# Kernel optimization log

Hardware: AMD Instinct MI355X
Metric: run time of the kernel (lower is better)

The kernel has to match this reference:

```python
import jax, jax.numpy as jnp
import numpy as np


def setup_inputs() -> dict:
    B, C, D = 8192, 2048, 1024
    key = jax.random.key(0)
    kx, kc = jax.random.split(key)
    x = jax.random.normal(kx, (B, D), dtype=jnp.float32)
    # kaiming_normal_ init for centers: std = sqrt(2 / fan_in) with fan_in = feat_dim
    centers = jax.random.normal(kc, (C, D), dtype=jnp.float32) * jnp.sqrt(2.0 / D)
    sigma = jnp.ones((C, D), dtype=jnp.float32)  # nn.init.ones_
    return {"x": x, "centers": centers, "sigma": sigma}


def reference(x, centers, sigma):
    # Original loop computes, per class i:
    #   dist[:, i] = diag(m @ diag(sigma[i]) @ m.T)  with m = x - centers[i]
    # which equals sum_d sigma[i,d] * (x[b,d] - centers[i,d])^2.
    # Expand the square to avoid the O(B*C*D) broadcast intermediate:
    #   dist[b,i] = (x^2) @ sigma[i] - 2 * x @ (sigma[i]*centers[i]) + sum_d sigma[i,d]*centers[i,d]^2
    xsq_term = jnp.einsum('bd,id->bi', x * x, sigma)            # [B, C]
    cross = jnp.einsum('bd,id->bi', x, sigma * centers)          # [B, C]
    const = jnp.sum(sigma * centers * centers, axis=-1)          # [C]
    dist = xsq_term - 2.0 * cross + const[None, :]
    return (centers, sigma, -dist)
```

## Files before the change

### kernel.cpp

```cpp
#include <hip/hip_runtime.h>
#include <hip/hip_bf16.h>


#define B_SZ 8192
#define C_SZ 2048
#define D_SZ 1024
#define K2   2048
#define NT   32

typedef __attribute__((ext_vector_type(4))) float f32x4;
typedef __attribute__((ext_vector_type(8))) short bf16x8;

static __device__ __forceinline__ unsigned short f2bf(float f) {
  union { float f; unsigned int u; } v; v.f = f;
  unsigned int r = v.u + 0x7fffu + ((v.u >> 16) & 1u);
  return (unsigned short)(r >> 16);
}

__global__ __launch_bounds__(256) void build_a(const float* __restrict__ x,
                                               unsigned short* __restrict__ Aop) {
  const long t = (long)blockIdx.x * 256 + threadIdx.x;
  const long e = t * 8;
  const long b = e >> 10;
  const int  d = (int)(e & 1023);
  const float4* xv = (const float4*)x;
  float4 v0 = xv[2 * t], v1 = xv[2 * t + 1];
  float vs[8] = {v0.x, v0.y, v0.z, v0.w, v1.x, v1.y, v1.z, v1.w};
  unsigned short sq[8] __attribute__((aligned(16)));
  unsigned short rw[8] __attribute__((aligned(16)));
#pragma unroll
  for (int j = 0; j < 8; ++j) {
    rw[j] = f2bf(vs[j]);
    sq[j] = f2bf(vs[j] * vs[j]);
  }
  *(uint4*)(Aop + b * K2 + d)        = *(uint4*)sq;
  *(uint4*)(Aop + b * K2 + D_SZ + d) = *(uint4*)rw;
}

__global__ __launch_bounds__(128) void prep_w(const float* __restrict__ centers,
                                              const float* __restrict__ sigma,
                                              float* __restrict__ out_centers,
                                              float* __restrict__ out_sigma,
                                              unsigned short* __restrict__ Wop,
                                              float* __restrict__ cn) {
  const int i = blockIdx.x;
  const int t = threadIdx.x;
  const long base = (long)i * D_SZ;
  const float4* cv = (const float4*)(centers + base);
  const float4* sv = (const float4*)(sigma + base);
  float4 c0 = cv[2 * t], c1 = cv[2 * t + 1];
  float4 s0 = sv[2 * t], s1 = sv[2 * t + 1];
  ((float4*)(out_centers + base))[2 * t]     = c0;
  ((float4*)(out_centers + base))[2 * t + 1] = c1;
  ((float4*)(out_sigma + base))[2 * t]       = s0;
  ((float4*)(out_sigma + base))[2 * t + 1]   = s1;
  float cs[8] = {c0.x, c0.y, c0.z, c0.w, c1.x, c1.y, c1.z, c1.w};
  float ss[8] = {s0.x, s0.y, s0.z, s0.w, s1.x, s1.y, s1.z, s1.w};
  unsigned short w1[8] __attribute__((aligned(16)));
  unsigned short w2[8] __attribute__((aligned(16)));
  float p = 0.0f;
#pragma unroll
  for (int j = 0; j < 8; ++j) {
    w1[j] = f2bf(-ss[j]);
    w2[j] = f2bf(2.0f * ss[j] * cs[j]);
    p += ss[j] * cs[j] * cs[j];
  }
  *(uint4*)(Wop + (long)i * K2 + t * 8)        = *(uint4*)w1;
  *(uint4*)(Wop + (long)i * K2 + D_SZ + t * 8) = *(uint4*)w2;
#pragma unroll
  for (int off = 32; off > 0; off >>= 1) p += __shfl_down(p, off, 64);
  __shared__ float red[2];
  if ((t & 63) == 0) red[t >> 6] = p;
  __syncthreads();
  if (t == 0) cn[i] = -(red[0] + red[1]);
}

#define LGKM0() asm volatile("s_waitcnt lgkmcnt(0)" ::: "memory")
#define VM4()   asm volatile("s_waitcnt vmcnt(4)" ::: "memory")
#define VM0()   asm volatile("s_waitcnt vmcnt(0)" ::: "memory")
#define NOW()   ((void)0)
#define SB()    __builtin_amdgcn_sched_barrier(0)
#define BAR()   __builtin_amdgcn_s_barrier()

#define STAGE_A(C, H, KT)                                                       \
  do {                                                                          \
    __builtin_amdgcn_global_load_lds(                                           \
        (__attribute__((address_space(1))) void*)(aS + ((H)*128 + 0) * (long)K2 + (long)(KT)*64),  \
        (__attribute__((address_space(3))) void*)(&As[C][(H)*8192 + dstE]), 16, 0, 0);             \
    __builtin_amdgcn_global_load_lds(                                           \
        (__attribute__((address_space(1))) void*)(aS + ((H)*128 + 64) * (long)K2 + (long)(KT)*64), \
        (__attribute__((address_space(3))) void*)(&As[C][(H)*8192 + 4096 + dstE]), 16, 0, 0);      \
  } while (0)

#define STAGE_B(C, H, KT)                                                       \
  do {                                                                          \
    __builtin_amdgcn_global_load_lds(                                           \
        (__attribute__((address_space(1))) void*)(bS + ((H)*128 + 0) * (long)K2 + (long)(KT)*64),  \
        (__attribute__((address_space(3))) void*)(&Bs[C][(H)*8192 + dstE]), 16, 0, 0);             \
    __builtin_amdgcn_global_load_lds(                                           \
        (__attribute__((address_space(1))) void*)(bS + ((H)*128 + 64) * (long)K2 + (long)(KT)*64), \
        (__attribute__((address_space(3))) void*)(&Bs[C][(H)*8192 + 4096 + dstE]), 16, 0, 0);      \
  } while (0)

#define MM16(A0, A1, A2, A3, B0, B1, B2, B3, R)                                  \
  acc[(R)+0][0] = __builtin_amdgcn_mfma_f32_16x16x32_bf16(A0, B0, acc[(R)+0][0], 0,0,0); \
  acc[(R)+0][1] = __builtin_amdgcn_mfma_f32_16x16x32_bf16(A0, B1, acc[(R)+0][1], 0,0,0); \
  acc[(R)+0][2] = __builtin_amdgcn_mfma_f32_16x16x32_bf16(A0, B2, acc[(R)+0][2], 0,0,0); \
  acc[(R)+0][3] = __builtin_amdgcn_mfma_f32_16x16x32_bf16(A0, B3, acc[(R)+0][3], 0,0,0); \
  acc[(R)+1][0] = __builtin_amdgcn_mfma_f32_16x16x32_bf16(A1, B0, acc[(R)+1][0], 0,0,0); \
  acc[(R)+1][1] = __builtin_amdgcn_mfma_f32_16x16x32_bf16(A1, B1, acc[(R)+1][1], 0,0,0); \
  acc[(R)+1][2] = __builtin_amdgcn_mfma_f32_16x16x32_bf16(A1, B2, acc[(R)+1][2], 0,0,0); \
  acc[(R)+1][3] = __builtin_amdgcn_mfma_f32_16x16x32_bf16(A1, B3, acc[(R)+1][3], 0,0,0); \
  acc[(R)+2][0] = __builtin_amdgcn_mfma_f32_16x16x32_bf16(A2, B0, acc[(R)+2][0], 0,0,0); \
  acc[(R)+2][1] = __builtin_amdgcn_mfma_f32_16x16x32_bf16(A2, B1, acc[(R)+2][1], 0,0,0); \
  acc[(R)+2][2] = __builtin_amdgcn_mfma_f32_16x16x32_bf16(A2, B2, acc[(R)+2][2], 0,0,0); \
  acc[(R)+2][3] = __builtin_amdgcn_mfma_f32_16x16x32_bf16(A2, B3, acc[(R)+2][3], 0,0,0); \
  acc[(R)+3][0] = __builtin_amdgcn_mfma_f32_16x16x32_bf16(A3, B0, acc[(R)+3][0], 0,0,0); \
  acc[(R)+3][1] = __builtin_amdgcn_mfma_f32_16x16x32_bf16(A3, B1, acc[(R)+3][1], 0,0,0); \
  acc[(R)+3][2] = __builtin_amdgcn_mfma_f32_16x16x32_bf16(A3, B2, acc[(R)+3][2], 0,0,0); \
  acc[(R)+3][3] = __builtin_amdgcn_mfma_f32_16x16x32_bf16(A3, B3, acc[(R)+3][3], 0,0,0);

#define PH_TAIL()                                                              \
  SB(); BAR(); LGKM0(); SB(); __builtin_amdgcn_s_setprio(1)
#define PH_END()                                                               \
  __builtin_amdgcn_s_setprio(0); SB(); BAR()

#define TILE(C, U, STGA, STGB, BNDW)                                           \
  do {                                                                         \
    {                                          \
      bf16x8 a0 = *(const bf16x8*)(&As[C][aRd0 +    0]);                       \
      bf16x8 a1 = *(const bf16x8*)(&As[C][aRd0 + 1024]);                       \
      bf16x8 a2 = *(const bf16x8*)(&As[C][aRd0 + 2048]);                       \
      bf16x8 a3 = *(const bf16x8*)(&As[C][aRd0 + 3072]);                       \
      b00 = *(const bf16x8*)(&Bs[C][bRd0 +    0]);                             \
      b01 = *(const bf16x8*)(&Bs[C][bRd0 + 1024]);                             \
      b02 = *(const bf16x8*)(&Bs[C][bRd0 + 2048]);                             \
      b03 = *(const bf16x8*)(&Bs[C][bRd0 + 3072]);                             \
      if (STGA) STAGE_A((C)^1, 0, (U)+1);                                      \
      PH_TAIL();                                                               \
      MM16(a0, a1, a2, a3, b00, b01, b02, b03, 0)                              \
      PH_END();                                                                \
    }                                                                          \
    {                             \
      bf16x8 a0 = *(const bf16x8*)(&As[C][aRd0 + 4096]);                       \
      bf16x8 a1 = *(const bf16x8*)(&As[C][aRd0 + 5120]);                       \
      bf16x8 a2 = *(const bf16x8*)(&As[C][aRd0 + 6144]);                       \
      bf16x8 a3 = *(const bf16x8*)(&As[C][aRd0 + 7168]);                       \
      b10 = *(const bf16x8*)(&Bs[C][bRd1 +    0]);                             \
      b11 = *(const bf16x8*)(&Bs[C][bRd1 + 1024]);                             \
      b12 = *(const bf16x8*)(&Bs[C][bRd1 + 2048]);                             \
      b13 = *(const bf16x8*)(&Bs[C][bRd1 + 3072]);                             \
      if (STGA) STAGE_A((C)^1, 1, (U)+1);                                      \
      PH_TAIL();                                                               \
      MM16(a0, a1, a2, a3, b00, b01, b02, b03, 4)                              \
      PH_END();                                                                \
    }                                                                          \
    {                                          \
      bf16x8 a0 = *(const bf16x8*)(&As[C][aRd1 +    0]);                       \
      bf16x8 a1 = *(const bf16x8*)(&As[C][aRd1 + 1024]);                       \
      bf16x8 a2 = *(const bf16x8*)(&As[C][aRd1 + 2048]);                       \
      bf16x8 a3 = *(const bf16x8*)(&As[C][aRd1 + 3072]);                       \
      if (STGB) STAGE_B((C), 0, (U)+2);                                        \
      PH_TAIL();                                                               \
      MM16(a0, a1, a2, a3, b10, b11, b12, b13, 0)                              \
      PH_END();                                                                \
    }                                                                          \
    {                                \
      bf16x8 a0 = *(const bf16x8*)(&As[C][aRd1 + 4096]);                       \
      bf16x8 a1 = *(const bf16x8*)(&As[C][aRd1 + 5120]);                       \
      bf16x8 a2 = *(const bf16x8*)(&As[C][aRd1 + 6144]);                       \
      bf16x8 a3 = *(const bf16x8*)(&As[C][aRd1 + 7168]);                       \
      if (STGB) STAGE_B((C), 1, (U)+2);                                        \
      PH_TAIL();                                                               \
      MM16(a0, a1, a2, a3, b10, b11, b12, b13, 4)                              \
      __builtin_amdgcn_s_setprio(0);                                           \
      BNDW(); SB(); BAR();                                                     \
    }                                                                          \
  } while (0)

__global__ __launch_bounds__(512, 2) void gemm256(const unsigned short* __restrict__ A,
                                                  const unsigned short* __restrict__ W,
                                                  const float* __restrict__ cn,
                                                  float* __restrict__ out) {
  __shared__ __attribute__((aligned(16))) unsigned short As[2][16384];
  __shared__ __attribute__((aligned(16))) unsigned short Bs[2][16384];

  const int tid  = threadIdx.x;
  const int lane = tid & 63;
  const int wave = tid >> 6;
  const int wr = wave >> 2;
  const int wc = wave & 3;

  const int bid = blockIdx.x;
  const int xcd = bid & 7, idx = bid >> 3;
  const long rowBase = (long)(xcd * 4 + (idx >> 3)) * 256;
  const long colBase = (long)(idx & 7) * 256;

  const int sr = tid >> 3;
  const int sl = (tid & 7) ^ (sr & 7);
  const unsigned short* aS = A + (rowBase + sr) * (long)K2 + sl * 8;
  const unsigned short* bS = W + (colBase + sr) * (long)K2 + sl * 8;
  const int dstE = tid * 8;

  const int l15 = lane & 15, l7 = lane & 7, q = lane >> 4;
  const int ps0 = q ^ l7;
  const int ps1 = ps0 ^ 4;
  const int aRd0 = (wr * 128 + l15) * 64 + ps0 * 8;
  const int aRd1 = (wr * 128 + l15) * 64 + ps1 * 8;
  const int bRd0 = (wc * 64 + l15) * 64 + ps0 * 8;
  const int bRd1 = (wc * 64 + l15) * 64 + ps1 * 8;

  f32x4 acc[8][4];
#pragma unroll
  for (int i = 0; i < 8; ++i)
#pragma unroll
    for (int j = 0; j < 4; ++j) acc[i][j] = (f32x4){0.f, 0.f, 0.f, 0.f};

  bf16x8 b00, b01, b02, b03, b10, b11, b12, b13;

  STAGE_A(0, 0, 0); STAGE_A(0, 1, 0);
  STAGE_B(0, 0, 0); STAGE_B(0, 1, 0);
  STAGE_B(1, 0, 1); STAGE_B(1, 1, 1);
  VM4(); SB(); BAR();

#pragma unroll 1
  for (int u = 0; u < 28; u += 2) {
    TILE(0, u,     1, 1, VM4);
    TILE(1, u + 1, 1, 1, VM4);
  }
  TILE(0, 28, 1, 1, VM4);
  TILE(1, 29, 1, 1, VM4);
  TILE(0, 30, 1, 0, VM0);
  TILE(1, 31, 0, 0, NOW);

  const int crow = (lane >> 4) * 4;
  const int ccol = lane & 15;
#pragma unroll
  for (int ni = 0; ni < 4; ++ni) {
    const long col = colBase + wc * 64 + ni * 16 + ccol;
    const float c = cn[col];
#pragma unroll
    for (int mi = 0; mi < 8; ++mi) {
      const long row = rowBase + wr * 128 + mi * 16 + crow;
      float* o = out + row * C_SZ + col;
#pragma unroll
      for (int j = 0; j < 4; ++j) o[(long)j * C_SZ] = acc[mi][ni][j] + c;
    }
  }
}

extern "C" void kernel_launch(void* const* d_in, const int* in_sizes, int n_in,
                              void* d_out, int out_size, void* d_ws, size_t ws_size,
                              hipStream_t stream) {
  const float* x       = (const float*)d_in[0];
  const float* centers = (const float*)d_in[1];
  const float* sigma   = (const float*)d_in[2];
  float* out = (float*)d_out;

  unsigned short* Aop = (unsigned short*)d_ws;
  unsigned short* Wop = Aop + (long)B_SZ * K2;
  float* cnp = (float*)(Wop + (long)C_SZ * K2);

  build_a<<<B_SZ * D_SZ / 8 / 256, 256, 0, stream>>>(x, Aop);
  prep_w<<<C_SZ, 128, 0, stream>>>(centers, sigma,
                                   out, out + (size_t)C_SZ * D_SZ, Wop, cnp);

  float* out2 = out + (size_t)2 * C_SZ * D_SZ;
  gemm256<<<256, 512, 0, stream>>>(Aop, Wop, cnp, out2);
}
```

Before: 86.69 us.

## Load B fragments directly from global to registers, triple-buffer A in LDS

B-operand fragments are no longer staged through LDS. Each wave now loads its own B slice from global memory straight into a double-buffered register array (bE/bO) one k-tile ahead. The freed LDS goes to a third A buffer, so A prefetch runs two tiles ahead, with vmcnt waits adjusted to match. This removes the B LDS writes and reads and their bank traffic. In exchange it costs more VGPRs, uncoalesced per-wave global loads of B that duplicate traffic across the two wave rows, and a risk to occupancy at two blocks per CU.

```diff
diff --git a/kernel.cpp b/kernel.cpp
--- a/kernel.cpp
+++ b/kernel.cpp
@@ -6,7 +6,6 @@
 #define C_SZ 2048
 #define D_SZ 1024
 #define K2   2048
-#define NT   32
 
 typedef __attribute__((ext_vector_type(4))) float f32x4;
 typedef __attribute__((ext_vector_type(8))) short bf16x8;
@@ -76,8 +75,8 @@
 }
 
 #define LGKM0() asm volatile("s_waitcnt lgkmcnt(0)" ::: "memory")
-#define VM4()   asm volatile("s_waitcnt vmcnt(4)" ::: "memory")
-#define VM0()   asm volatile("s_waitcnt vmcnt(0)" ::: "memory")
+#define VM12()  asm volatile("s_waitcnt vmcnt(12)" ::: "memory")
+#define VM8()   asm volatile("s_waitcnt vmcnt(8)" ::: "memory")
 #define NOW()   ((void)0)
 #define SB()    __builtin_amdgcn_sched_barrier(0)
 #define BAR()   __builtin_amdgcn_s_barrier()
@@ -92,15 +91,11 @@
         (__attribute__((address_space(3))) void*)(&As[C][(H)*8192 + 4096 + dstE]), 16, 0, 0);      \
   } while (0)
 
-#define STAGE_B(C, H, KT)                                                       \
-  do {                                                                          \
-    __builtin_amdgcn_global_load_lds(                                           \
-        (__attribute__((address_space(1))) void*)(bS + ((H)*128 + 0) * (long)K2 + (long)(KT)*64),  \
-        (__attribute__((address_space(3))) void*)(&Bs[C][(H)*8192 + dstE]), 16, 0, 0);             \
-    __builtin_amdgcn_global_load_lds(                                           \
-        (__attribute__((address_space(1))) void*)(bS + ((H)*128 + 64) * (long)K2 + (long)(KT)*64), \
-        (__attribute__((address_space(3))) void*)(&Bs[C][(H)*8192 + 4096 + dstE]), 16, 0, 0);      \
-  } while (0)
+#define LOADB(DST, T, KK)                                                       \
+  DST[(KK)*4+0] = *(const bf16x8*)(bG + 0*(long)K2*16 + (long)(T)*64 + (KK)*32);\
+  DST[(KK)*4+1] = *(const bf16x8*)(bG + 1*(long)K2*16 + (long)(T)*64 + (KK)*32);\
+  DST[(KK)*4+2] = *(const bf16x8*)(bG + 2*(long)K2*16 + (long)(T)*64 + (KK)*32);\
+  DST[(KK)*4+3] = *(const bf16x8*)(bG + 3*(long)K2*16 + (long)(T)*64 + (KK)*32);
 
 #define MM16(A0, A1, A2, A3, B0, B1, B2, B3, R)                                  \
   acc[(R)+0][0] = __builtin_amdgcn_mfma_f32_16x16x32_bf16(A0, B0, acc[(R)+0][0], 0,0,0); \
@@ -125,54 +120,46 @@
 #define PH_END()                                                               \
   __builtin_amdgcn_s_setprio(0); SB(); BAR()
 
-#define TILE(C, U, STGA, STGB, BNDW)                                           \
+#define TILE(AC, SC, BC, BN, U, STGA, LDB, BNDW)                               \
   do {                                                                         \
     {                                          \
-      bf16x8 a0 = *(const bf16x8*)(&As[C][aRd0 +    0]);                       \
-      bf16x8 a1 = *(const bf16x8*)(&As[C][aRd0 + 1024]);                       \
-      bf16x8 a2 = *(const bf16x8*)(&As[C][aRd0 + 2048]);                       \
-      bf16x8 a3 = *(const bf16x8*)(&As[C][aRd0 + 3072]);                       \
-      b00 = *(const bf16x8*)(&Bs[C][bRd0 +    0]);                             \
-      b01 = *(const bf16x8*)(&Bs[C][bRd0 + 1024]);                             \
-      b02 = *(const bf16x8*)(&Bs[C][bRd0 + 2048]);                             \
-      b03 = *(const bf16x8*)(&Bs[C][bRd0 + 3072]);                             \
-      if (STGA) STAGE_A((C)^1, 0, (U)+1);                                      \
-      PH_TAIL();                                                               \
-      MM16(a0, a1, a2, a3, b00, b01, b02, b03, 0)                              \
+      bf16x8 a0 = *(const bf16x8*)(&As[AC][aRd0 +    0]);                      \
+      bf16x8 a1 = *(const bf16x8*)(&As[AC][aRd0 + 1024]);                      \
+      bf16x8 a2 = *(const bf16x8*)(&As[AC][aRd0 + 2048]);                      \
+      bf16x8 a3 = *(const bf16x8*)(&As[AC][aRd0 + 3072]);                      \
+      if (STGA) STAGE_A(SC, 0, (U)+2);                                         \
+      PH_TAIL();                                                               \
+      MM16(a0, a1, a2, a3, BC[0], BC[1], BC[2], BC[3], 0)                      \
       PH_END();                                                                \
     }                                                                          \
-    {                             \
-      bf16x8 a0 = *(const bf16x8*)(&As[C][aRd0 + 4096]);                       \
-      bf16x8 a1 = *(const bf16x8*)(&As[C][aRd0 + 5120]);                       \
-      bf16x8 a2 = *(const bf16x8*)(&As[C][aRd0 + 6144]);                       \
-      bf16x8 a3 = *(const bf16x8*)(&As[C][aRd0 + 7168]);                       \
-      b10 = *(const bf16x8*)(&Bs[C][bRd1 +    0]);                             \
-      b11 = *(const bf16x8*)(&Bs[C][bRd1 + 1024]);                             \
-      b12 = *(const bf16x8*)(&Bs[C][bRd1 + 2048]);                             \
-      b13 = *(const bf16x8*)(&Bs[C][bRd1 + 3072]);                             \
-      if (STGA) STAGE_A((C)^1, 1, (U)+1);                                      \
-      PH_TAIL();                                                               \
-      MM16(a0, a1, a2, a3, b00, b01, b02, b03, 4)                              \
+    {                                          \
+      bf16x8 a0 = *(const bf16x8*)(&As[AC][aRd0 + 4096]);                      \
+      bf16x8 a1 = *(const bf16x8*)(&As[AC][aRd0 + 5120]);                      \
+      bf16x8 a2 = *(const bf16x8*)(&As[AC][aRd0 + 6144]);                      \
+      bf16x8 a3 = *(const bf16x8*)(&As[AC][aRd0 + 7168]);                      \
+      if (LDB) { LOADB(BN, (U)+1, 0) }                                         \
+      PH_TAIL();                                                               \
+      MM16(a0, a1, a2, a3, BC[0], BC[1], BC[2], BC[3], 4)                      \
       PH_END();                                                                \
     }                                                                          \
     {                                          \
-      bf16x8 a0 = *(const bf16x8*)(&As[C][aRd1 +    0]);                       \
-      bf16x8 a1 = *(const bf16x8*)(&As[C][aRd1 + 1024]);                       \
-      bf16x8 a2 = *(const bf16x8*)(&As[C][aRd1 + 2048]);                       \
-      bf16x8 a3 = *(const bf16x8*)(&As[C][aRd1 + 3072]);                       \
-      if (STGB) STAGE_B((C), 0, (U)+2);                                        \
-      PH_TAIL();                                                               \
-      MM16(a0, a1, a2, a3, b10, b11, b12, b13, 0)                              \
+      bf16x8 a0 = *(const bf16x8*)(&As[AC][aRd1 +    0]);                      \
+      bf16x8 a1 = *(const bf16x8*)(&As[AC][aRd1 + 1024]);                      \
+      bf16x8 a2 = *(const bf16x8*)(&As[AC][aRd1 + 2048]);                      \
+      bf16x8 a3 = *(const bf16x8*)(&As[AC][aRd1 + 3072]);                      \
+      if (STGA) STAGE_A(SC, 1, (U)+2);                                         \
+      PH_TAIL();                                                               \
+      MM16(a0, a1, a2, a3, BC[4], BC[5], BC[6], BC[7], 0)                      \
       PH_END();                                                                \
     }                                                                          \
     {                                \
-      bf16x8 a0 = *(const bf16x8*)(&As[C][aRd1 + 4096]);                       \
-      bf16x8 a1 = *(const bf16x8*)(&As[C][aRd1 + 5120]);                       \
-      bf16x8 a2 = *(const bf16x8*)(&As[C][aRd1 + 6144]);                       \
-      bf16x8 a3 = *(const bf16x8*)(&As[C][aRd1 + 7168]);                       \
-      if (STGB) STAGE_B((C), 1, (U)+2);                                        \
-      PH_TAIL();                                                               \
-      MM16(a0, a1, a2, a3, b10, b11, b12, b13, 4)                              \
+      bf16x8 a0 = *(const bf16x8*)(&As[AC][aRd1 + 4096]);                      \
+      bf16x8 a1 = *(const bf16x8*)(&As[AC][aRd1 + 5120]);                      \
+      bf16x8 a2 = *(const bf16x8*)(&As[AC][aRd1 + 6144]);                      \
+      bf16x8 a3 = *(const bf16x8*)(&As[AC][aRd1 + 7168]);                      \
+      if (LDB) { LOADB(BN, (U)+1, 1) }                                         \
+      PH_TAIL();                                                               \
+      MM16(a0, a1, a2, a3, BC[4], BC[5], BC[6], BC[7], 4)                      \
       __builtin_amdgcn_s_setprio(0);                                           \
       BNDW(); SB(); BAR();                                                     \
     }                                                                          \
@@ -182,8 +169,7 @@
                                                   const unsigned short* __restrict__ W,
                                                   const float* __restrict__ cn,
                                                   float* __restrict__ out) {
-  __shared__ __attribute__((aligned(16))) unsigned short As[2][16384];
-  __shared__ __attribute__((aligned(16))) unsigned short Bs[2][16384];
+  __shared__ __attribute__((aligned(16))) unsigned short As[3][16384];
 
   const int tid  = threadIdx.x;
   const int lane = tid & 63;
@@ -199,7 +185,6 @@
   const int sr = tid >> 3;
   const int sl = (tid & 7) ^ (sr & 7);
   const unsigned short* aS = A + (rowBase + sr) * (long)K2 + sl * 8;
-  const unsigned short* bS = W + (colBase + sr) * (long)K2 + sl * 8;
   const int dstE = tid * 8;
 
   const int l15 = lane & 15, l7 = lane & 7, q = lane >> 4;
@@ -207,8 +192,8 @@
   const int ps1 = ps0 ^ 4;
   const int aRd0 = (wr * 128 + l15) * 64 + ps0 * 8;
   const int aRd1 = (wr * 128 + l15) * 64 + ps1 * 8;
-  const int bRd0 = (wc * 64 + l15) * 64 + ps0 * 8;
-  const int bRd1 = (wc * 64 + l15) * 64 + ps1 * 8;
+
+  const unsigned short* bG = W + (colBase + wc * 64 + l15) * (long)K2 + q * 8;
 
   f32x4 acc[8][4];
 #pragma unroll
@@ -216,22 +201,25 @@
 #pragma unroll
     for (int j = 0; j < 4; ++j) acc[i][j] = (f32x4){0.f, 0.f, 0.f, 0.f};
 
-  bf16x8 b00, b01, b02, b03, b10, b11, b12, b13;
+  bf16x8 bE[8], bO[8];
 
   STAGE_A(0, 0, 0); STAGE_A(0, 1, 0);
-  STAGE_B(0, 0, 0); STAGE_B(0, 1, 0);
-  STAGE_B(1, 0, 1); STAGE_B(1, 1, 1);
-  VM4(); SB(); BAR();
+  STAGE_A(1, 0, 1); STAGE_A(1, 1, 1);
+  LOADB(bE, 0, 0) LOADB(bE, 0, 1)
+  VM12();
+  SB(); BAR();
 
 #pragma unroll 1
-  for (int u = 0; u < 28; u += 2) {
-    TILE(0, u,     1, 1, VM4);
-    TILE(1, u + 1, 1, 1, VM4);
-  }
-  TILE(0, 28, 1, 1, VM4);
-  TILE(1, 29, 1, 1, VM4);
-  TILE(0, 30, 1, 0, VM0);
-  TILE(1, 31, 0, 0, NOW);
+  for (int u = 0; u < 30; u += 6) {
+    TILE(0, 2, bE, bO, u + 0, 1, 1, VM12);
+    TILE(1, 0, bO, bE, u + 1, 1, 1, VM12);
+    TILE(2, 1, bE, bO, u + 2, 1, 1, VM12);
+    TILE(0, 2, bO, bE, u + 3, 1, 1, VM12);
+    TILE(1, 0, bE, bO, u + 4, 1, 1, VM12);
+    TILE(2, 1, bO, bE, u + 5, 1, 1, VM12);
+  }
+  TILE(0, 2, bE, bO, 30, 0, 1, VM8);
+  TILE(1, 0, bO, bE, 31, 0, 0, NOW);
 
   const int crow = (lane >> 4) * 4;
   const int ccol = lane & 15;
```

Result: slower. 115.8 us (+33.5%).
